# Performance work log

Measured on AMD Instinct MI355X. Metric: run time of the kernel, lower is better.

Reference implementation:

```python
import jax, jax.numpy as jnp
import numpy as np

B, S, E, H, D = 4, 2048, 1024, 16, 64  # batch, seq, embed, heads, head_dim


def setup_inputs() -> dict:
    key = jax.random.key(0)
    k1, k2, k3 = jax.random.split(key, 3)
    x = jax.random.normal(k1, (B, S, E), dtype=jnp.float32)
    qkv_w = jax.random.normal(k2, (E, H, 3 * D), dtype=jnp.float32) * (1.0 / np.sqrt(E))
    qkv_b = jnp.zeros((H, 3 * D), dtype=jnp.float32)
    out_w = jax.random.normal(k3, (H, D, E), dtype=jnp.float32) * (1.0 / np.sqrt(H * D))
    out_b = jnp.zeros((E,), dtype=jnp.float32)
    return {"x": x, "qkv_w": qkv_w, "qkv_b": qkv_b, "out_w": out_w, "out_b": out_b}


def _large_negative_number(dtype):
    return jnp.asarray(-0.7 * jnp.finfo(dtype).max, dtype=dtype)


def reference(x, qkv_w, qkv_b, out_w, out_b):
    # qkv projection: LinearGeneral(E -> (H, 3D))
    qkv = jnp.einsum('bse,ehd->bshd', x, qkv_w) + qkv_b  # [B,S,H,3D]
    q, k, v = jnp.split(qkv, 3, axis=-1)  # each [B,S,H,D]
    logits = jnp.einsum('bqhd,bkhd->bhqk', q, k)  # [B,H,S,S]
    logits = logits / jnp.sqrt(jnp.asarray(q.shape[-1], logits.dtype))
    mask = jnp.tril(jnp.ones((q.shape[1], q.shape[1]), dtype=jnp.bool_))
    logits = jnp.where(mask, logits, _large_negative_number(logits.dtype))
    probs = jax.nn.softmax(logits, axis=-1)
    attn = jnp.einsum('bhqk,bkhd->bqhd', probs, v)  # [B,S,H,D]
    # output projection: LinearGeneral((H, D) -> E)
    return jnp.einsum('bqhd,hde->bqe', attn, out_w) + out_b
```

## Files before the change

kernel.cpp:

```cpp
#include <hip/hip_runtime.h>

typedef unsigned int u32;
typedef _Float16 f16;
typedef _Float16 f16x8 __attribute__((ext_vector_type(8)));
typedef _Float16 f16x4 __attribute__((ext_vector_type(4)));
typedef float f32x4 __attribute__((ext_vector_type(4)));

#define LOG2E 1.4426950408889634f

__device__ __forceinline__ void gl_lds16(const void* g, void* l) {
  __builtin_amdgcn_global_load_lds(
      (const __attribute__((address_space(1))) u32*)g,
      (__attribute__((address_space(3))) u32*)l, 16, 0, 0);
}

__device__ __forceinline__ f32x4 mfma16(f16x8 a, f16x8 b, f32x4 c) {
  return __builtin_amdgcn_mfma_f32_16x16x32_f16(a, b, c, 0, 0, 0);
}

__global__ void k_cvt(const float* __restrict__ in, f16* __restrict__ out, int n4) {
  int stride = gridDim.x * blockDim.x;
  for (int i = blockIdx.x * blockDim.x + threadIdx.x; i < n4; i += stride) {
    f32x4 v = *(const f32x4*)(in + (size_t)i * 4);
    f16x4 o;
    o[0] = (f16)v[0]; o[1] = (f16)v[1]; o[2] = (f16)v[2]; o[3] = (f16)v[3];
    *(f16x4*)(out + (size_t)i * 4) = o;
  }
}

__global__ void k_tconv(const float* __restrict__ in, f16* __restrict__ out, int R, int C) {
  __shared__ f16 tile[32][33];
  int c0 = blockIdx.x * 32, r0 = blockIdx.y * 32;
  int tx = threadIdx.x, ty = threadIdx.y;
#pragma unroll
  for (int i = ty; i < 32; i += 8)
    tile[i][tx] = (f16)in[(size_t)(r0 + i) * C + c0 + tx];
  __syncthreads();
#pragma unroll
  for (int i = ty; i < 32; i += 8)
    out[(size_t)(c0 + i) * R + r0 + tx] = tile[tx][i];
}

__device__ __forceinline__ void gemm_fat(
    const f16* __restrict__ A, const f16* __restrict__ Bt,
    int bm, int bn, f16* SM, int w, int lane, f32x4 (&acc)[8][4]) {
  constexpr int KT = 32;
  const int g = lane >> 4, rl = lane & 15;
  const int l4 = lane >> 2, ls = lane & 3;
  const int sslot = ls ^ ((l4 >> 1) & 3);

  const f16* aS = A + (size_t)(bm + w * 32 + l4) * 1024 + sslot * 8;
  const f16* bS = Bt + (size_t)(bn + w * 16 + l4) * 1024 + sslot * 8;
  f16* aD = SM + w * 1024;
  f16* bD = SM + 4096 + w * 512;

#define STGH0(b, kt) do { \
    gl_lds16(aS + (kt) * 32,          aD + (b) * 12288); \
    gl_lds16(aS + 16384 + (kt) * 32,  aD + (b) * 12288 + 512); \
    gl_lds16(bS + (kt) * 32,          bD + (b) * 12288); } while (0)
#define STGH1(b, kt) do { \
    gl_lds16(bS + 65536 + (kt) * 32,  bD + (b) * 12288 + 2048); \
    gl_lds16(bS + 131072 + (kt) * 32, bD + (b) * 12288 + 4096); \
    gl_lds16(bS + 196608 + (kt) * 32, bD + (b) * 12288 + 6144); } while (0)

  STGH0(0, 0); STGH1(0, 0);
  STGH0(1, 1); STGH1(1, 1);
  asm volatile("s_waitcnt vmcnt(6)" ::: "memory");
  __builtin_amdgcn_s_barrier();

  const int ro = rl * 32 + ((g ^ ((rl >> 1) & 3)) * 8);

  int c = 0, cs = 2;
#pragma unroll 1
  for (int kt = 0; kt < KT; ++kt) {
    const f16* SMc = SM + c * 12288;
    const bool stg = (kt + 2 < KT);
    f16x8 bf[4], af[4];

    {
#pragma unroll
      for (int j = 0; j < 4; ++j)
        bf[j] = *(const f16x8*)(SMc + 4096 + w * 2048 + j * 512 + ro);
#pragma unroll
      for (int mi = 0; mi < 4; ++mi)
        af[mi] = *(const f16x8*)(SMc + mi * 512 + ro);
      if (stg) STGH0(cs, kt + 2);
      __builtin_amdgcn_s_barrier();
      asm volatile("s_waitcnt lgkmcnt(0)" ::: "memory");
      __builtin_amdgcn_sched_barrier(0);
      __builtin_amdgcn_s_setprio(1);
#pragma unroll
      for (int mi = 0; mi < 4; ++mi)
#pragma unroll
        for (int j = 0; j < 4; ++j)
          acc[mi][j] = mfma16(af[mi], bf[j], acc[mi][j]);
      __builtin_amdgcn_s_setprio(0);
      __builtin_amdgcn_sched_barrier(0);
      __builtin_amdgcn_s_barrier();
    }

    {
#pragma unroll
      for (int mi = 0; mi < 4; ++mi)
        af[mi] = *(const f16x8*)(SMc + (4 + mi) * 512 + ro);
      if (stg) STGH1(cs, kt + 2);
      __builtin_amdgcn_s_barrier();
      asm volatile("s_waitcnt lgkmcnt(0)" ::: "memory");
      __builtin_amdgcn_sched_barrier(0);
      __builtin_amdgcn_s_setprio(1);
#pragma unroll
      for (int mi = 0; mi < 4; ++mi)
#pragma unroll
        for (int j = 0; j < 4; ++j)
          acc[4 + mi][j] = mfma16(af[mi], bf[j], acc[4 + mi][j]);
      __builtin_amdgcn_s_setprio(0);
      __builtin_amdgcn_sched_barrier(0);
      if (kt + 2 < KT)      { asm volatile("s_waitcnt vmcnt(6)" ::: "memory"); }
      else if (kt + 1 < KT) { asm volatile("s_waitcnt vmcnt(0)" ::: "memory"); }
      __builtin_amdgcn_s_barrier();
      __builtin_amdgcn_sched_barrier(0);
    }

    c = (c == 2) ? 0 : c + 1;
    cs = (cs == 2) ? 0 : cs + 1;
  }
#undef STGH0
#undef STGH1
}

__global__ __launch_bounds__(256, 2) void k_gemm_qkv4(
    const f16* __restrict__ A, const f16* __restrict__ Bt,
    const float* __restrict__ bias,
    f16* __restrict__ qo, f16* __restrict__ ko2, f16* __restrict__ vto) {
  __shared__ __align__(16) f16 SM[36864];
  const int lin0 = blockIdx.y * 12 + blockIdx.x;
  const int lin = (lin0 & 7) * 96 + (lin0 >> 3);
  const int bn = (lin % 12) * 256, bm = (lin / 12) * 128;
  const int t = threadIdx.x, lane = t & 63, w = t >> 6;
  const int g = lane >> 4, rl = lane & 15;

  f32x4 acc[8][4] = {};
  gemm_fat(A, Bt, bm, bn, SM, w, lane, acc);

#pragma unroll
  for (int mi = 0; mi < 8; ++mi)
#pragma unroll
    for (int j = 0; j < 4; ++j)
#pragma unroll
      for (int r = 0; r < 4; ++r) {
        int m = bm + mi * 16 + g * 4 + r;
        int n = bn + w * 64 + j * 16 + rl;
        float v = acc[mi][j][r] + bias[n];
        int b = m >> 11, s = m & 2047;
        int h = n / 192, rem = n - h * 192;
        int tsel = rem >> 6, d = rem & 63;
        size_t bh = (size_t)(b * 16 + h);
        if (tsel == 0)      qo[(bh * 2048 + s) * 64 + d] = (f16)(v * (0.125f * LOG2E));
        else if (tsel == 1) ko2[(bh * 2048 + s) * 64 + d] = (f16)v;
        else                vto[(bh * 64 + d) * 2048 + s] = (f16)v;
      }
}

__global__ __launch_bounds__(256, 2) void k_gemm_out4(
    const f16* __restrict__ A, const f16* __restrict__ Bt,
    const float* __restrict__ bias, float* __restrict__ out) {
  __shared__ __align__(16) f16 SM[36864];
  const int lin0 = blockIdx.y * 4 + blockIdx.x;
  const int lin = (lin0 & 7) * 32 + (lin0 >> 3);
  const int bn = (lin % 4) * 256, bm = (lin / 4) * 128;
  const int t = threadIdx.x, lane = t & 63, w = t >> 6;
  const int g = lane >> 4, rl = lane & 15;

  f32x4 acc[8][4] = {};
  gemm_fat(A, Bt, bm, bn, SM, w, lane, acc);

#pragma unroll
  for (int mi = 0; mi < 8; ++mi)
#pragma unroll
    for (int j = 0; j < 4; ++j)
#pragma unroll
      for (int r = 0; r < 4; ++r) {
        int m = bm + mi * 16 + g * 4 + r;
        int n = bn + w * 64 + j * 16 + rl;
        out[(size_t)m * 1024 + n] = acc[mi][j][r] + bias[n];
      }
}

__global__ __launch_bounds__(256, 4) void k_attn2(
    const f16* __restrict__ q, const f16* __restrict__ kgl,
    const f16* __restrict__ vt, f16* __restrict__ o) {
  constexpr int S = 2048;
  __shared__ __align__(16) f16 Ks[2][64 * 64];
  __shared__ __align__(16) f16 Vs[2][64 * 64];
  __shared__ __align__(16) f16 Ps[4][16 * 64];

  const int blk = blockIdx.x;
  const int sidx = blk >> 3;
  const int bh = (blk & 7) * 8 + (sidx & 7);
  const int qb = 15 - (sidx >> 3);

  const int t = threadIdx.x, lane = t & 63, w = t >> 6;
  const int g = lane >> 4, rl = lane & 15;

  const f16* qp = q + ((size_t)bh * S + qb * 128) * 64;
  const f16* kb = kgl + (size_t)bh * S * 64;
  const f16* vb = vt + (size_t)bh * 64 * S;

  f16x8 qf[2][2];
#pragma unroll
  for (int sub = 0; sub < 2; ++sub)
#pragma unroll
    for (int ks = 0; ks < 2; ++ks)
      qf[sub][ks] = *(const f16x8*)(qp + (size_t)(w * 32 + sub * 16 + rl) * 64 + ks * 32 + g * 8);

  f32x4 oacc[2][4] = {};
  float lrow[2] = {0.f, 0.f};

  const int srow = lane >> 3;
  const int sslot = (lane & 7) ^ srow;

  const int nkt = 2 * qb + 2;
  const int qmaxw = qb * 128 + w * 32 + 31;

  auto STAGE = [&](int bufi, int kt) {
#pragma unroll
    for (int i = 0; i < 2; ++i) {
      const int r0 = w * 16 + i * 8;
      gl_lds16(kb + (size_t)(kt * 64 + r0 + srow) * 64 + sslot * 8, &Ks[bufi][r0 * 64]);
      gl_lds16(vb + (size_t)(r0 + srow) * S + kt * 64 + sslot * 8, &Vs[bufi][r0 * 64]);
    }
  };

  STAGE(0, 0);
  __syncthreads();
  int buf = 0;

  for (int kt = 0; kt < nkt; ++kt) {
    if (kt + 1 < nkt) STAGE(buf ^ 1, kt + 1);

    if (kt * 64 <= qmaxw) {
      const f16* Kb = &Ks[buf][0];
      const f16* Vb = &Vs[buf][0];
#pragma unroll
      for (int sub = 0; sub < 2; ++sub) {
        const int qsub = qb * 128 + w * 32 + sub * 16;
        if (kt * 64 > qsub + 15) continue;

        f32x4 sT[4] = {};
#pragma unroll
        for (int j = 0; j < 4; ++j)
#pragma unroll
          for (int ks = 0; ks < 2; ++ks) {
            int row = j * 16 + rl;
            f16x8 kf = *(const f16x8*)(Kb + row * 64 + (((ks * 4 + g) ^ (rl & 7)) * 8));
            sT[j] = mfma16(kf, qf[sub][ks], sT[j]);
          }

        if (kt * 64 + 63 > qsub) {
#pragma unroll
          for (int j = 0; j < 4; ++j)
#pragma unroll
            for (int r = 0; r < 4; ++r)
              if (kt * 64 + j * 16 + g * 4 + r > qsub + rl) sT[j][r] = -1e30f;
        }

        float ps = 0.f;
#pragma unroll
        for (int j = 0; j < 4; ++j) {
          f16x4 pb;
#pragma unroll
          for (int r = 0; r < 4; ++r) {
            float p = exp2f(sT[j][r]);
            ps += p;
            pb[r] = (f16)p;
          }
          *(f16x4*)(&Ps[w][0] + rl * 64 + (((j * 2 + (g >> 1)) ^ (rl & 7)) * 8) + (g & 1) * 4) = pb;
        }
        lrow[sub] += ps;

        asm volatile("s_waitcnt lgkmcnt(0)" ::: "memory");
        __builtin_amdgcn_sched_barrier(0);

        f16x8 pf[2];
#pragma unroll
        for (int ks = 0; ks < 2; ++ks)
          pf[ks] = *(const f16x8*)(&Ps[w][0] + rl * 64 + (((ks * 4 + g) ^ (rl & 7)) * 8));

#pragma unroll
        for (int dj = 0; dj < 4; ++dj)
#pragma unroll
          for (int ks = 0; ks < 2; ++ks) {
            int vrow = dj * 16 + rl;
            f16x8 vf = *(const f16x8*)(Vb + vrow * 64 + (((ks * 4 + g) ^ (rl & 7)) * 8));
            oacc[sub][dj] = mfma16(pf[ks], vf, oacc[sub][dj]);
          }
      }
    }
    __syncthreads();
    buf ^= 1;
  }

  float rinv[2];
#pragma unroll
  for (int sub = 0; sub < 2; ++sub) {
    float s_ = lrow[sub];
    s_ += __shfl_xor(s_, 16, 64);
    s_ += __shfl_xor(s_, 32, 64);
    rinv[sub] = 1.0f / s_;
  }

  const int h = bh & 15;
  const size_t rowb = (size_t)(bh >> 4) * 2048 + qb * 128 + w * 32;
#pragma unroll
  for (int sub = 0; sub < 2; ++sub)
#pragma unroll
    for (int r = 0; r < 4; ++r) {
      float ri = __shfl(rinv[sub], g * 4 + r, 64);
#pragma unroll
      for (int dj = 0; dj < 4; ++dj)
        o[(rowb + sub * 16 + g * 4 + r) * 1024 + h * 64 + dj * 16 + rl] =
            (f16)(oacc[sub][dj][r] * ri);
    }
}

extern "C" void kernel_launch(void* const* d_in, const int* in_sizes, int n_in,
                              void* d_out, int out_size, void* d_ws, size_t ws_size,
                              hipStream_t stream) {
  (void)in_sizes; (void)n_in; (void)out_size; (void)ws_size;
  const float* x    = (const float*)d_in[0];
  const float* wqkv = (const float*)d_in[1];
  const float* bqkv = (const float*)d_in[2];
  const float* wo   = (const float*)d_in[3];
  const float* bo   = (const float*)d_in[4];
  float* out = (float*)d_out;
  char* ws = (char*)d_ws;

  f16* xb    = (f16*)(ws + 0);
  f16* wqkvt = (f16*)(ws + 16777216);
  f16* wot   = (f16*)(ws + 23068672);
  f16* qws   = (f16*)(ws + 25165824);
  f16* kws   = (f16*)(ws + 41943040);
  f16* vtws  = (f16*)(ws + 58720256);
  f16* attnb = xb;

  k_cvt<<<2048, 256, 0, stream>>>(x, xb, 8388608 / 4);
  k_tconv<<<dim3(96, 32), dim3(32, 8), 0, stream>>>(wqkv, wqkvt, 1024, 3072);
  k_tconv<<<dim3(32, 32), dim3(32, 8), 0, stream>>>(wo, wot, 1024, 1024);
  k_gemm_qkv4<<<dim3(12, 64), 256, 0, stream>>>(xb, wqkvt, bqkv, qws, kws, vtws);
  k_attn2<<<1024, 256, 0, stream>>>(qws, kws, vtws, attnb);
  k_gemm_out4<<<dim3(4, 64), 256, 0, stream>>>(attnb, wot, bo, out);
}
```

Measured before the change: 191.2 us.

## Load K/V directly from global in attention, drop LDS staging and block syncs

The attention kernel no longer stages K and V tiles into shared memory with double buffering and __syncthreads. Each wave now reads K and V fragments straight from global memory (relying on cache) and processes both 16-row query subtiles together, sharing each K/V fragment across two MFMAs. This also lets each wave run its own causal loop length instead of the block-wide maximum. The QKV GEMM is split into a copy that uses inline-asm ds_read_b128 LDS loads and a drop of the memory clobber on the wait, while the output GEMM keeps the old code. The trade is more global/L2 traffic and exposed load latency in attention, plus a risk of reordering LDS reads in the GEMM.

Result: slower. 272.7 us (+42.6%).

```diff
diff --git a/kernel.cpp b/kernel.cpp
--- a/kernel.cpp
+++ b/kernel.cpp
@@ -5,6 +5,7 @@
 typedef _Float16 f16x8 __attribute__((ext_vector_type(8)));
 typedef _Float16 f16x4 __attribute__((ext_vector_type(4)));
 typedef float f32x4 __attribute__((ext_vector_type(4)));
+typedef _Float16 __attribute__((address_space(3))) lf16;
 
 #define LOG2E 1.4426950408889634f
 
@@ -16,6 +17,12 @@
 
 __device__ __forceinline__ f32x4 mfma16(f16x8 a, f16x8 b, f32x4 c) {
   return __builtin_amdgcn_mfma_f32_16x16x32_f16(a, b, c, 0, 0, 0);
+}
+
+__device__ __forceinline__ f16x8 ldsr(const f16* p) {
+  f16x8 r;
+  asm volatile("ds_read_b128 %0, %1" : "=v"(r) : "v"((const lf16*)p));
+  return r;
 }
 
 __global__ void k_cvt(const float* __restrict__ in, f16* __restrict__ out, int n4) {
@@ -41,7 +48,7 @@
     out[(size_t)(c0 + i) * R + r0 + tx] = tile[tx][i];
 }
 
-__device__ __forceinline__ void gemm_fat(
+__device__ __forceinline__ void gemm_fatA(
     const f16* __restrict__ A, const f16* __restrict__ Bt,
     int bm, int bn, f16* SM, int w, int lane, f32x4 (&acc)[8][4]) {
   constexpr int KT = 32;
@@ -54,17 +61,17 @@
   f16* aD = SM + w * 1024;
   f16* bD = SM + 4096 + w * 512;
 
-#define STGH0(b, kt) do { \
+#define ASTG0(b, kt) do { \
     gl_lds16(aS + (kt) * 32,          aD + (b) * 12288); \
     gl_lds16(aS + 16384 + (kt) * 32,  aD + (b) * 12288 + 512); \
     gl_lds16(bS + (kt) * 32,          bD + (b) * 12288); } while (0)
-#define STGH1(b, kt) do { \
+#define ASTG1(b, kt) do { \
     gl_lds16(bS + 65536 + (kt) * 32,  bD + (b) * 12288 + 2048); \
     gl_lds16(bS + 131072 + (kt) * 32, bD + (b) * 12288 + 4096); \
     gl_lds16(bS + 196608 + (kt) * 32, bD + (b) * 12288 + 6144); } while (0)
 
-  STGH0(0, 0); STGH1(0, 0);
-  STGH0(1, 1); STGH1(1, 1);
+  ASTG0(0, 0); ASTG1(0, 0);
+  ASTG0(1, 1); ASTG1(1, 1);
   asm volatile("s_waitcnt vmcnt(6)" ::: "memory");
   __builtin_amdgcn_s_barrier();
 
@@ -80,13 +87,13 @@
     {
 #pragma unroll
       for (int j = 0; j < 4; ++j)
-        bf[j] = *(const f16x8*)(SMc + 4096 + w * 2048 + j * 512 + ro);
-#pragma unroll
-      for (int mi = 0; mi < 4; ++mi)
-        af[mi] = *(const f16x8*)(SMc + mi * 512 + ro);
-      if (stg) STGH0(cs, kt + 2);
-      __builtin_amdgcn_s_barrier();
-      asm volatile("s_waitcnt lgkmcnt(0)" ::: "memory");
+        bf[j] = ldsr(SMc + 4096 + w * 2048 + j * 512 + ro);
+#pragma unroll
+      for (int mi = 0; mi < 4; ++mi)
+        af[mi] = ldsr(SMc + mi * 512 + ro);
+      if (stg) ASTG0(cs, kt + 2);
+      __builtin_amdgcn_s_barrier();
+      asm volatile("s_waitcnt lgkmcnt(0)");
       __builtin_amdgcn_sched_barrier(0);
       __builtin_amdgcn_s_setprio(1);
 #pragma unroll
@@ -102,10 +109,10 @@
     {
 #pragma unroll
       for (int mi = 0; mi < 4; ++mi)
-        af[mi] = *(const f16x8*)(SMc + (4 + mi) * 512 + ro);
-      if (stg) STGH1(cs, kt + 2);
-      __builtin_amdgcn_s_barrier();
-      asm volatile("s_waitcnt lgkmcnt(0)" ::: "memory");
+        af[mi] = ldsr(SMc + (4 + mi) * 512 + ro);
+      if (stg) ASTG1(cs, kt + 2);
+      __builtin_amdgcn_s_barrier();
+      asm volatile("s_waitcnt lgkmcnt(0)");
       __builtin_amdgcn_sched_barrier(0);
       __builtin_amdgcn_s_setprio(1);
 #pragma unroll
@@ -124,8 +131,92 @@
     c = (c == 2) ? 0 : c + 1;
     cs = (cs == 2) ? 0 : cs + 1;
   }
-#undef STGH0
-#undef STGH1
+#undef ASTG0
+#undef ASTG1
+}
+
+__device__ __forceinline__ void gemm_fatC(
+    const f16* __restrict__ A, const f16* __restrict__ Bt,
+    int bm, int bn, f16* SM, int w, int lane, f32x4 (&acc)[8][4]) {
+  constexpr int KT = 32;
+  const int g = lane >> 4, rl = lane & 15;
+  const int l4 = lane >> 2, ls = lane & 3;
+  const int sslot = ls ^ ((l4 >> 1) & 3);
+
+  const f16* aS = A + (size_t)(bm + w * 32 + l4) * 1024 + sslot * 8;
+  const f16* bS = Bt + (size_t)(bn + w * 16 + l4) * 1024 + sslot * 8;
+  f16* aD = SM + w * 1024;
+  f16* bD = SM + 4096 + w * 512;
+
+#define CSTG0(b, kt) do { \
+    gl_lds16(aS + (kt) * 32,          aD + (b) * 12288); \
+    gl_lds16(aS + 16384 + (kt) * 32,  aD + (b) * 12288 + 512); \
+    gl_lds16(bS + (kt) * 32,          bD + (b) * 12288); } while (0)
+#define CSTG1(b, kt) do { \
+    gl_lds16(bS + 65536 + (kt) * 32,  bD + (b) * 12288 + 2048); \
+    gl_lds16(bS + 131072 + (kt) * 32, bD + (b) * 12288 + 4096); \
+    gl_lds16(bS + 196608 + (kt) * 32, bD + (b) * 12288 + 6144); } while (0)
+
+  CSTG0(0, 0); CSTG1(0, 0);
+  CSTG0(1, 1); CSTG1(1, 1);
+  asm volatile("s_waitcnt vmcnt(6)" ::: "memory");
+  __builtin_amdgcn_s_barrier();
+
+  const int ro = rl * 32 + ((g ^ ((rl >> 1) & 3)) * 8);
+
+  int c = 0, cs = 2;
+#pragma unroll 1
+  for (int kt = 0; kt < KT; ++kt) {
+    const f16* SMc = SM + c * 12288;
+    const bool stg = (kt + 2 < KT);
+    f16x8 bf[4], af[4];
+    {
+#pragma unroll
+      for (int j = 0; j < 4; ++j)
+        bf[j] = *(const f16x8*)(SMc + 4096 + w * 2048 + j * 512 + ro);
+#pragma unroll
+      for (int mi = 0; mi < 4; ++mi)
+        af[mi] = *(const f16x8*)(SMc + mi * 512 + ro);
+      if (stg) CSTG0(cs, kt + 2);
+      __builtin_amdgcn_s_barrier();
+      asm volatile("s_waitcnt lgkmcnt(0)" ::: "memory");
+      __builtin_amdgcn_sched_barrier(0);
+      __builtin_amdgcn_s_setprio(1);
+#pragma unroll
+      for (int mi = 0; mi < 4; ++mi)
+#pragma unroll
+        for (int j = 0; j < 4; ++j)
+          acc[mi][j] = mfma16(af[mi], bf[j], acc[mi][j]);
+      __builtin_amdgcn_s_setprio(0);
+      __builtin_amdgcn_sched_barrier(0);
+      __builtin_amdgcn_s_barrier();
+    }
+    {
+#pragma unroll
+      for (int mi = 0; mi < 4; ++mi)
+        af[mi] = *(const f16x8*)(SMc + (4 + mi) * 512 + ro);
+      if (stg) CSTG1(cs, kt + 2);
+      __builtin_amdgcn_s_barrier();
+      asm volatile("s_waitcnt lgkmcnt(0)" ::: "memory");
+      __builtin_amdgcn_sched_barrier(0);
+      __builtin_amdgcn_s_setprio(1);
+#pragma unroll
+      for (int mi = 0; mi < 4; ++mi)
+#pragma unroll
+        for (int j = 0; j < 4; ++j)
+          acc[4 + mi][j] = mfma16(af[mi], bf[j], acc[4 + mi][j]);
+      __builtin_amdgcn_s_setprio(0);
+      __builtin_amdgcn_sched_barrier(0);
+      if (kt + 2 < KT)      { asm volatile("s_waitcnt vmcnt(6)" ::: "memory"); }
+      else if (kt + 1 < KT) { asm volatile("s_waitcnt vmcnt(0)" ::: "memory"); }
+      __builtin_amdgcn_s_barrier();
+      __builtin_amdgcn_sched_barrier(0);
+    }
+    c = (c == 2) ? 0 : c + 1;
+    cs = (cs == 2) ? 0 : cs + 1;
+  }
+#undef CSTG0
+#undef CSTG1
 }
 
 __global__ __launch_bounds__(256, 2) void k_gemm_qkv4(
@@ -140,7 +231,7 @@
   const int g = lane >> 4, rl = lane & 15;
 
   f32x4 acc[8][4] = {};
-  gemm_fat(A, Bt, bm, bn, SM, w, lane, acc);
+  gemm_fatA(A, Bt, bm, bn, SM, w, lane, acc);
 
 #pragma unroll
   for (int mi = 0; mi < 8; ++mi)
@@ -172,7 +263,7 @@
   const int g = lane >> 4, rl = lane & 15;
 
   f32x4 acc[8][4] = {};
-  gemm_fat(A, Bt, bm, bn, SM, w, lane, acc);
+  gemm_fatC(A, Bt, bm, bn, SM, w, lane, acc);
 
 #pragma unroll
   for (int mi = 0; mi < 8; ++mi)
@@ -190,9 +281,7 @@
     const f16* __restrict__ q, const f16* __restrict__ kgl,
     const f16* __restrict__ vt, f16* __restrict__ o) {
   constexpr int S = 2048;
-  __shared__ __align__(16) f16 Ks[2][64 * 64];
-  __shared__ __align__(16) f16 Vs[2][64 * 64];
-  __shared__ __align__(16) f16 Ps[4][16 * 64];
+  __shared__ __align__(16) f16 Ps[4][32 * 64];
 
   const int blk = blockIdx.x;
   const int sidx = blk >> 3;
@@ -216,88 +305,72 @@
   f32x4 oacc[2][4] = {};
   float lrow[2] = {0.f, 0.f};
 
-  const int srow = lane >> 3;
-  const int sslot = (lane & 7) ^ srow;
-
-  const int nkt = 2 * qb + 2;
-  const int qmaxw = qb * 128 + w * 32 + 31;
-
-  auto STAGE = [&](int bufi, int kt) {
-#pragma unroll
-    for (int i = 0; i < 2; ++i) {
-      const int r0 = w * 16 + i * 8;
-      gl_lds16(kb + (size_t)(kt * 64 + r0 + srow) * 64 + sslot * 8, &Ks[bufi][r0 * 64]);
-      gl_lds16(vb + (size_t)(r0 + srow) * S + kt * 64 + sslot * 8, &Vs[bufi][r0 * 64]);
-    }
-  };
-
-  STAGE(0, 0);
-  __syncthreads();
-  int buf = 0;
-
-  for (int kt = 0; kt < nkt; ++kt) {
-    if (kt + 1 < nkt) STAGE(buf ^ 1, kt + 1);
-
-    if (kt * 64 <= qmaxw) {
-      const f16* Kb = &Ks[buf][0];
-      const f16* Vb = &Vs[buf][0];
+  const f16* kRow = kb + (size_t)rl * 64 + g * 8;
+  const f16* vRow = vb + (size_t)rl * 2048 + g * 8;
+
+  const int qsub0 = qb * 128 + w * 32;
+  const int nktw = ((qsub0 + 31) >> 6) + 1;
+
+  for (int kt = 0; kt < nktw; ++kt) {
+    f32x4 sT[2][4] = {};
+#pragma unroll
+    for (int j = 0; j < 4; ++j)
+#pragma unroll
+      for (int ks = 0; ks < 2; ++ks) {
+        f16x8 kf = *(const f16x8*)(kRow + (size_t)(kt * 64 + j * 16) * 64 + ks * 32);
+        sT[0][j] = mfma16(kf, qf[0][ks], sT[0][j]);
+        sT[1][j] = mfma16(kf, qf[1][ks], sT[1][j]);
+      }
+
+    if (kt * 64 + 63 > qsub0) {
 #pragma unroll
       for (int sub = 0; sub < 2; ++sub) {
-        const int qsub = qb * 128 + w * 32 + sub * 16;
-        if (kt * 64 > qsub + 15) continue;
-
-        f32x4 sT[4] = {};
+        const int qs = qsub0 + sub * 16;
 #pragma unroll
         for (int j = 0; j < 4; ++j)
 #pragma unroll
-          for (int ks = 0; ks < 2; ++ks) {
-            int row = j * 16 + rl;
-            f16x8 kf = *(const f16x8*)(Kb + row * 64 + (((ks * 4 + g) ^ (rl & 7)) * 8));
-            sT[j] = mfma16(kf, qf[sub][ks], sT[j]);
-          }
-
-        if (kt * 64 + 63 > qsub) {
-#pragma unroll
-          for (int j = 0; j < 4; ++j)
-#pragma unroll
-            for (int r = 0; r < 4; ++r)
-              if (kt * 64 + j * 16 + g * 4 + r > qsub + rl) sT[j][r] = -1e30f;
+          for (int r = 0; r < 4; ++r)
+            if (kt * 64 + j * 16 + g * 4 + r > qs + rl) sT[sub][j][r] = -1e30f;
+      }
+    }
+
+#pragma unroll
+    for (int sub = 0; sub < 2; ++sub) {
+      float ps = 0.f;
+#pragma unroll
+      for (int j = 0; j < 4; ++j) {
+        f16x4 pb;
+#pragma unroll
+        for (int r = 0; r < 4; ++r) {
+          float p = exp2f(sT[sub][j][r]);
+          ps += p;
+          pb[r] = (f16)p;
         }
-
-        float ps = 0.f;
-#pragma unroll
-        for (int j = 0; j < 4; ++j) {
-          f16x4 pb;
-#pragma unroll
-          for (int r = 0; r < 4; ++r) {
-            float p = exp2f(sT[j][r]);
-            ps += p;
-            pb[r] = (f16)p;
-          }
-          *(f16x4*)(&Ps[w][0] + rl * 64 + (((j * 2 + (g >> 1)) ^ (rl & 7)) * 8) + (g & 1) * 4) = pb;
-        }
-        lrow[sub] += ps;
-
-        asm volatile("s_waitcnt lgkmcnt(0)" ::: "memory");
-        __builtin_amdgcn_sched_barrier(0);
-
-        f16x8 pf[2];
-#pragma unroll
-        for (int ks = 0; ks < 2; ++ks)
-          pf[ks] = *(const f16x8*)(&Ps[w][0] + rl * 64 + (((ks * 4 + g) ^ (rl & 7)) * 8));
-
-#pragma unroll
-        for (int dj = 0; dj < 4; ++dj)
-#pragma unroll
-          for (int ks = 0; ks < 2; ++ks) {
-            int vrow = dj * 16 + rl;
-            f16x8 vf = *(const f16x8*)(Vb + vrow * 64 + (((ks * 4 + g) ^ (rl & 7)) * 8));
-            oacc[sub][dj] = mfma16(pf[ks], vf, oacc[sub][dj]);
-          }
-      }
-    }
-    __syncthreads();
-    buf ^= 1;
+        *(f16x4*)(&Ps[w][0] + (sub * 16 + rl) * 64 +
+                  (((j * 2 + (g >> 1)) ^ (rl & 7)) * 8) + (g & 1) * 4) = pb;
+      }
+      lrow[sub] += ps;
+    }
+
+    asm volatile("s_waitcnt lgkmcnt(0)" ::: "memory");
+    __builtin_amdgcn_sched_barrier(0);
+
+    f16x8 pf[2][2];
+#pragma unroll
+    for (int sub = 0; sub < 2; ++sub)
+#pragma unroll
+      for (int ks = 0; ks < 2; ++ks)
+        pf[sub][ks] = *(const f16x8*)(&Ps[w][0] + (sub * 16 + rl) * 64 +
+                                      (((ks * 4 + g) ^ (rl & 7)) * 8));
+
+#pragma unroll
+    for (int dj = 0; dj < 4; ++dj)
+#pragma unroll
+      for (int ks = 0; ks < 2; ++ks) {
+        f16x8 vf = *(const f16x8*)(vRow + (size_t)(dj * 16) * 2048 + kt * 64 + ks * 32);
+        oacc[0][dj] = mfma16(pf[0][ks], vf, oacc[0][dj]);
+        oacc[1][dj] = mfma16(pf[1][ks], vf, oacc[1][dj]);
+      }
   }
 
   float rinv[2];
```
